# Kernel tuning notes

Hardware: AMD Instinct MI355X
Metric: run time of the kernel (lower is better)

The kernel has to match this reference:

```python
import jax, jax.numpy as jnp
import numpy as np

D_STATE = 16

def setup_inputs() -> dict:
    key = jax.random.key(0)
    ks = jax.random.split(key, 7)
    B, L, d_model = 2, 4096, 1024
    d_inner, d_conv, d_state = 2048, 4, D_STATE
    s = 0.02
    return {
        "x": jax.random.normal(ks[0], (B, L, d_model), jnp.float32),
        "W_in": jax.random.normal(ks[1], (2 * d_inner, d_model), jnp.float32) * s,
        "conv_w": jax.random.normal(ks[2], (d_inner, d_conv), jnp.float32) * 0.3,
        "conv_b": jax.random.normal(ks[3], (d_inner,), jnp.float32) * 0.1,
        "W_xproj": jax.random.normal(ks[4], (2 * d_state + d_inner, d_inner), jnp.float32) * s,
        "D": jnp.ones((d_inner,), jnp.float32),
        "W_out": jax.random.normal(ks[5], (d_model, d_inner), jnp.float32) * s,
    }

def _silu(v):
    return v * jax.nn.sigmoid(v)

def reference(x, W_in, conv_w, conv_b, W_xproj, D, W_out):
    Bsz, L, _ = x.shape
    d_inner, d_conv = conv_w.shape
    d_state = D_STATE
    # in_proj -> split into x branch and gate z
    xz = jnp.einsum('bld,ed->ble', x, W_in)           # [B,L,2*d_inner]
    xb, z = xz[..., :d_inner], xz[..., d_inner:]
    # causal depthwise conv1d (left pad d_conv-1, truncate to L)
    xpad = jnp.pad(xb, ((0, 0), (d_conv - 1, 0), (0, 0)))
    xc = conv_b
    for k in range(d_conv):  # tiny fixed kernel loop
        xc = xc + conv_w[:, k] * xpad[:, k:k + L, :]
    xc = _silu(xc)                                    # [B,L,d_inner]
    # x_proj -> B, C, delta
    proj = jnp.einsum('bld,ed->ble', xc, W_xproj)     # [B,L,2*d_state+d_inner]
    Bm = proj[..., :d_state]
    Cm = proj[..., d_state:2 * d_state]
    delta = jax.nn.softplus(proj[..., 2 * d_state:])  # [B,L,d_inner]
    # selective 'scan' as written collapses: y[b,l,d] = delta*x * sum_s B*C + D*x
    bc = jnp.einsum('bls,bls->bl', Bm, Cm)            # [B,L]
    y = delta * xc * bc[..., None] + D * xc
    y = y * _silu(z)
    return jnp.einsum('bld,ed->ble', y, W_out)        # [B,L,d_model]
```

## Files before the change

### kernel.cpp

```cpp
#include <hip/hip_runtime.h>
#include <hip/hip_bf16.h>
#include <cstdint>
#include <cmath>

typedef __bf16 bf16x8 __attribute__((ext_vector_type(8)));
typedef float  f32x4  __attribute__((ext_vector_type(4)));
typedef unsigned short u16x8 __attribute__((ext_vector_type(8)));

#define BT 128
#define BK 64

__device__ __forceinline__ float bf2f(unsigned short h) {
  union { unsigned int u; float f; } v; v.u = ((unsigned int)h) << 16;
  return v.f;
}
__device__ __forceinline__ unsigned short f2bf(float x) {
  union { float f; unsigned int u; } v; v.f = x;
  unsigned int r = v.u + 0x7fffu + ((v.u >> 16) & 1u);
  return (unsigned short)(r >> 16);
}

__device__ __forceinline__ void gld_lds16(const void* g, void* l) {
  __builtin_amdgcn_global_load_lds(
      (const __attribute__((address_space(1))) unsigned int*)g,
      (__attribute__((address_space(3))) unsigned int*)l,
      16, 0, 0);
}

__device__ __forceinline__ void cvt4(const float* __restrict__ in,
                                     unsigned short* __restrict__ out, int i) {
  float4 v = reinterpret_cast<const float4*>(in)[i];
  ushort4 o;
  o.x = f2bf(v.x); o.y = f2bf(v.y); o.z = f2bf(v.z); o.w = f2bf(v.w);
  reinterpret_cast<ushort4*>(out)[i] = o;
}

__global__ void cvt_head(const float* __restrict__ x, unsigned short* __restrict__ xb,
                         const float* __restrict__ W_in, unsigned short* __restrict__ wb) {
  int b = blockIdx.x;
  if (b < 8192) cvt4(x, xb, b * 256 + threadIdx.x);
  else          cvt4(W_in, wb, (b - 8192) * 256 + threadIdx.x);
}

__device__ void conv_strip(const unsigned short* __restrict__ xz,
                           const float* __restrict__ conv_w,
                           const float* __restrict__ conv_b,
                           unsigned short* __restrict__ xc,
                           int strip, int tid) {
  const int bl0  = strip * 32;
  const int seq0 = bl0 & ~4095;
  const int c0   = tid * 8;
  float w[4][8], bb[8];
#pragma unroll
  for (int j = 0; j < 8; ++j) {
    float4 wr = reinterpret_cast<const float4*>(conv_w)[c0 + j];
    w[0][j] = wr.x; w[1][j] = wr.y; w[2][j] = wr.z; w[3][j] = wr.w;
    bb[j] = conv_b[c0 + j];
  }
  float win[3][8];
#pragma unroll
  for (int i = 0; i < 3; ++i) {
    int r = bl0 - 3 + i;
    if (r >= seq0) {
      u16x8 v = *reinterpret_cast<const u16x8*>(xz + (size_t)r * 4096 + c0);
#pragma unroll
      for (int j = 0; j < 8; ++j) win[i][j] = bf2f(v[j]);
    } else {
#pragma unroll
      for (int j = 0; j < 8; ++j) win[i][j] = 0.f;
    }
  }
  for (int i = 0; i < 32; ++i) {
    const int bl = bl0 + i;
    u16x8 v = *reinterpret_cast<const u16x8*>(xz + (size_t)bl * 4096 + c0);
    u16x8 o;
#pragma unroll
    for (int j = 0; j < 8; ++j) {
      float cur = bf2f(v[j]);
      float a = bb[j] + w[0][j] * win[0][j] + w[1][j] * win[1][j]
                      + w[2][j] * win[2][j] + w[3][j] * cur;
      o[j] = f2bf(a / (1.f + __expf(-a)));
      win[0][j] = win[1][j]; win[1][j] = win[2][j]; win[2][j] = cur;
    }
    *reinterpret_cast<u16x8*>(xc + (size_t)bl * 2048 + c0) = o;
  }
}

__global__ void mid_fused(const unsigned short* __restrict__ xz,
                          const float* __restrict__ conv_w,
                          const float* __restrict__ conv_b,
                          unsigned short* __restrict__ xc,
                          const float* __restrict__ W_xproj, unsigned short* __restrict__ wx_bf,
                          const float* __restrict__ W_out,   unsigned short* __restrict__ wo_bf) {
  int b = blockIdx.x;
  if (b < 256) { conv_strip(xz, conv_w, conv_b, xc, b, threadIdx.x); return; }
  b -= 256;
  if (b < 4160) { cvt4(W_xproj, wx_bf, b * 256 + threadIdx.x); return; }
  cvt4(W_out, wo_bf, (b - 4160) * 256 + threadIdx.x);
}

template <int GUARD_N, int OUT_F32>
__global__ __launch_bounds__(256, 2)
void gemm_bt(const unsigned short* __restrict__ A,
             const unsigned short* __restrict__ B,
             void* __restrict__ Cv,
             int N, int K, int ldA, int ldB, int ldC)
{
  __shared__ __align__(16) unsigned short sA[BT * BK];
  __shared__ __align__(16) unsigned short sB[BT * BK];

  const int tid  = threadIdx.x;
  const int lane = tid & 63;
  const int wave = tid >> 6;
  const int row0 = blockIdx.x * BT;
  const int col0 = blockIdx.y * BT;

  const int wrow = (wave & 1) * 64;
  const int wcol = (wave >> 1) * 64;
  const int l15  = lane & 15;
  const int q    = lane >> 4;

  f32x4 acc[4][4];
#pragma unroll
  for (int i = 0; i < 4; ++i)
#pragma unroll
    for (int j = 0; j < 4; ++j)
      acc[i][j] = (f32x4){0.f, 0.f, 0.f, 0.f};

  const int nk = K / BK;
  for (int kt = 0; kt < nk; ++kt) {
    const int k0 = kt * BK;
#pragma unroll
    for (int t = 0; t < 4; ++t) {
      int c  = t * 256 + tid;
      int r  = c >> 3;
      int g  = c & 7;
      int gs = (g ^ (r & 7)) * 8;
      gld_lds16(A + (size_t)(row0 + r) * ldA + k0 + gs, (void*)(sA + c * 8));
      int br = col0 + r;
      if (GUARD_N) br = (br < N) ? br : (N - 1);
      gld_lds16(B + (size_t)br * ldB + k0 + gs, (void*)(sB + c * 8));
    }
    __syncthreads();

#pragma unroll
    for (int kk = 0; kk < BK; kk += 32) {
      const int grb = kk >> 3;
      bf16x8 af[4], bfr[4];
#pragma unroll
      for (int i = 0; i < 4; ++i) {
        int ar = wrow + i * 16 + l15;
        af[i] = *reinterpret_cast<const bf16x8*>(
            sA + ar * BK + (((grb + q) ^ (ar & 7)) << 3));
        int br = wcol + i * 16 + l15;
        bfr[i] = *reinterpret_cast<const bf16x8*>(
            sB + br * BK + (((grb + q) ^ (br & 7)) << 3));
      }
#pragma unroll
      for (int i = 0; i < 4; ++i)
#pragma unroll
        for (int j = 0; j < 4; ++j)
          acc[i][j] = __builtin_amdgcn_mfma_f32_16x16x32_bf16(af[i], bfr[j], acc[i][j], 0, 0, 0);
    }
    __syncthreads();
  }

#pragma unroll
  for (int i = 0; i < 4; ++i) {
#pragma unroll
    for (int j = 0; j < 4; ++j) {
      int colw = col0 + wcol + j * 16 + l15;
      if (GUARD_N && colw >= N) continue;
#pragma unroll
      for (int r = 0; r < 4; ++r) {
        int roww = row0 + wrow + i * 16 + q * 4 + r;
        if (OUT_F32)
          ((float*)Cv)[(size_t)roww * ldC + colw] = acc[i][j][r];
        else
          ((unsigned short*)Cv)[(size_t)roww * ldC + colw] = f2bf(acc[i][j][r]);
      }
    }
  }
}

#define BARX() do { __builtin_amdgcn_sched_barrier(0); \
                    __builtin_amdgcn_s_barrier(); \
                    __builtin_amdgcn_sched_barrier(0); } while (0)
#define VMW(n) asm volatile("s_waitcnt vmcnt(" #n ")" ::: "memory")
#define LGKM0() asm volatile("s_waitcnt lgkmcnt(0)" ::: "memory")

#define STAGE_A(b, h, kt) do { \
  const unsigned short* _p = Ab + (size_t)((h) * 128) * ldA + (kt) * 64; \
  gld_lds16(_p,                     (void*)&sA[b][((h) * 128      + rr) * 64 + (g8 << 3)]); \
  gld_lds16(_p + (size_t)64 * ldA,  (void*)&sA[b][((h) * 128 + 64 + rr) * 64 + (g8 << 3)]); \
} while (0)

#define STAGE_B(b, h, kt) do { \
  const unsigned short* _p = Bb + (size_t)((h) * 128) * ldB + (kt) * 64; \
  gld_lds16(_p,                     (void*)&sB[b][((h) * 128      + rr) * 64 + (g8 << 3)]); \
  gld_lds16(_p + (size_t)64 * ldB,  (void*)&sB[b][((h) * 128 + 64 + rr) * 64 + (g8 << 3)]); \
} while (0)

#define RD_A_SET(dst, b, p) do { \
  dst[0][0] = *reinterpret_cast<const bf16x8*>(&sA[b][aOff + (2*(p)    ) * 1024 + kph0]); \
  dst[0][1] = *reinterpret_cast<const bf16x8*>(&sA[b][aOff + (2*(p)    ) * 1024 + kph1]); \
  dst[1][0] = *reinterpret_cast<const bf16x8*>(&sA[b][aOff + (2*(p) + 1) * 1024 + kph0]); \
  dst[1][1] = *reinterpret_cast<const bf16x8*>(&sA[b][aOff + (2*(p) + 1) * 1024 + kph1]); \
} while (0)

#define RD_B_SET(dst, b) do { \
  dst[0][0] = *reinterpret_cast<const bf16x8*>(&sB[b][bOff + 0 * 1024 + kph0]); \
  dst[0][1] = *reinterpret_cast<const bf16x8*>(&sB[b][bOff + 0 * 1024 + kph1]); \
  dst[1][0] = *reinterpret_cast<const bf16x8*>(&sB[b][bOff + 1 * 1024 + kph0]); \
  dst[1][1] = *reinterpret_cast<const bf16x8*>(&sB[b][bOff + 1 * 1024 + kph1]); \
  dst[2][0] = *reinterpret_cast<const bf16x8*>(&sB[b][bOff + 2 * 1024 + kph0]); \
  dst[2][1] = *reinterpret_cast<const bf16x8*>(&sB[b][bOff + 2 * 1024 + kph1]); \
  dst[3][0] = *reinterpret_cast<const bf16x8*>(&sB[b][bOff + 3 * 1024 + kph0]); \
  dst[3][1] = *reinterpret_cast<const bf16x8*>(&sB[b][bOff + 3 * 1024 + kph1]); \
} while (0)

#define MMA(i, j, k, Af, Bf) \
  acc[i][j] = __builtin_amdgcn_mfma_f32_16x16x32_bf16(Af[(i) & 1][k], Bf[j][k], acc[i][j], 0, 0, 0)

#define MFMA_PH(p, Af, Bf) do { \
  __builtin_amdgcn_s_setprio(1); \
  MMA(2*(p),   0, 0, Af, Bf); MMA(2*(p),   1, 0, Af, Bf); \
  MMA(2*(p),   2, 0, Af, Bf); MMA(2*(p),   3, 0, Af, Bf); \
  MMA(2*(p)+1, 0, 0, Af, Bf); MMA(2*(p)+1, 1, 0, Af, Bf); \
  MMA(2*(p)+1, 2, 0, Af, Bf); MMA(2*(p)+1, 3, 0, Af, Bf); \
  MMA(2*(p),   0, 1, Af, Bf); MMA(2*(p),   1, 1, Af, Bf); \
  MMA(2*(p),   2, 1, Af, Bf); MMA(2*(p),   3, 1, Af, Bf); \
  MMA(2*(p)+1, 0, 1, Af, Bf); MMA(2*(p)+1, 1, 1, Af, Bf); \
  MMA(2*(p)+1, 2, 1, Af, Bf); MMA(2*(p)+1, 3, 1, Af, Bf); \
  __builtin_amdgcn_s_setprio(0); \
} while (0)

__global__ __launch_bounds__(512, 2)
void gemm256(const unsigned short* __restrict__ A,
             const unsigned short* __restrict__ B,
             unsigned short* __restrict__ C,
             int K, int ldA, int ldB, int ldC, int ccsh)
{
  __shared__ __align__(16) unsigned short smem[4 * 256 * 64];
  unsigned short (*sA)[256 * 64] = (unsigned short (*)[256 * 64])smem;
  unsigned short (*sB)[256 * 64] = (unsigned short (*)[256 * 64])(smem + 2 * 256 * 64);

  const int tid  = threadIdx.x;
  const int lane = tid & 63;
  const int wave = tid >> 6;
  const int wm = wave >> 2;
  const int wn = wave & 3;
  const int l15 = lane & 15;
  const int q   = lane >> 4;

  const int nwg = gridDim.x;
  const int wg  = blockIdx.x;
  const int x   = wg & 7;
  const int c   = wg >> 3;
  const int CC  = 1 << ccsh;
  const int R   = (nwg >> 3) >> ccsh;
  const int row0 = ((x >> 1) * R + (c >> ccsh)) * 256;
  const int col0 = ((x & 1) * CC + (c & (CC - 1))) * 256;

  const int rr  = tid >> 3;
  const int g8  = tid & 7;
  const int gsw = ((g8 ^ (rr & 7)) << 3);
  const unsigned short* Ab = A + (size_t)(row0 + rr) * ldA + gsw;
  const unsigned short* Bb = B + (size_t)(col0 + rr) * ldB + gsw;

  const int aOff = (wm * 128 + l15) * 64;
  const int bOff = (wn * 64  + l15) * 64;
  const int a7   = l15 & 7;
  const int kph0 = ((q       ^ a7) << 3);
  const int kph1 = (((4 + q) ^ a7) << 3);

  f32x4 acc[8][4];
#pragma unroll
  for (int i = 0; i < 8; ++i)
#pragma unroll
    for (int j = 0; j < 4; ++j)
      acc[i][j] = (f32x4){0.f, 0.f, 0.f, 0.f};

  bf16x8 afe[2][2], afo[2][2];
  bf16x8 bfe[4][2], bfo[4][2];

  const int nk = K >> 6;
  STAGE_A(0, 0, 0); STAGE_A(0, 1, 0);
  STAGE_B(0, 0, 0); STAGE_B(0, 1, 0);
  STAGE_B(1, 0, 1); STAGE_B(1, 1, 1);
  VMW(4);
  BARX();
  RD_B_SET(bfe, 0); RD_A_SET(afe, 0, 0);

  const int niter = K >> 7;
  for (int it = 0; it < niter; ++it) {
    const int kt1 = 2 * it + 1;
    int ktE = 2 * it + 2; if (ktE > nk - 1) ktE = nk - 1;
    int ktO = 2 * it + 3; if (ktO > nk - 1) ktO = nk - 1;

    STAGE_A(1, 0, kt1);
    BARX();
    MFMA_PH(0, afe, bfe); RD_A_SET(afo, 0, 1);
    BARX();
    STAGE_A(1, 1, kt1);
    BARX();
    MFMA_PH(1, afo, bfe); RD_A_SET(afe, 0, 2);
    BARX();
    STAGE_B(0, 0, ktE);
    BARX();
    MFMA_PH(2, afe, bfe); RD_A_SET(afo, 0, 3);
    BARX();
    STAGE_B(0, 1, ktE);
    VMW(4);
    BARX();
    MFMA_PH(3, afo, bfe); RD_B_SET(bfo, 1); RD_A_SET(afe, 1, 0);
    BARX();

    STAGE_A(0, 0, ktE);
    BARX();
    MFMA_PH(0, afe, bfo); RD_A_SET(afo, 1, 1);
    BARX();
    STAGE_A(0, 1, ktE);
    BARX();
    MFMA_PH(1, afo, bfo); RD_A_SET(afe, 1, 2);
    BARX();
    STAGE_B(1, 0, ktO);
    BARX();
    MFMA_PH(2, afe, bfo); RD_A_SET(afo, 1, 3);
    BARX();
    STAGE_B(1, 1, ktO);
    VMW(4);
    BARX();
    MFMA_PH(3, afo, bfo); RD_B_SET(bfe, 0); RD_A_SET(afe, 0, 0);
    BARX();
  }

  VMW(0);
  LGKM0();
  BARX();
  {
    unsigned short* cs = smem;
#pragma unroll
    for (int i = 0; i < 8; ++i) {
      const int row = wm * 128 + i * 16 + q * 4;
#pragma unroll
      for (int j = 0; j < 4; ++j) {
        const int col = wn * 64 + j * 16 + l15;
#pragma unroll
        for (int r = 0; r < 4; ++r)
          cs[(row + r) * 256 + col] = f2bf(acc[i][j][r]);
      }
    }
    LGKM0();
    BARX();
#pragma unroll
    for (int s = 0; s < 16; ++s) {
      const int u   = s * 4096 + tid * 8;
      const int row = u >> 8;
      const int col = u & 255;
      u16x8 v = *reinterpret_cast<const u16x8*>(&cs[u]);
      *reinterpret_cast<u16x8*>(C + (size_t)(row0 + row) * ldC + col0 + col) = v;
    }
  }
}

__global__ __launch_bounds__(256)
void proj_strip(const unsigned short* __restrict__ xc,
                const unsigned short* __restrict__ wx,
                unsigned short* __restrict__ proj)
{
  __shared__ float red[4][32 * 32];
  const int tid  = threadIdx.x;
  const int lane = tid & 63;
  const int wave = tid >> 6;
  const int l15  = lane & 15;
  const int q    = lane >> 4;
  const int row0 = blockIdx.x * 32;

  f32x4 acc[2][2];
#pragma unroll
  for (int i = 0; i < 2; ++i)
#pragma unroll
    for (int j = 0; j < 2; ++j) acc[i][j] = (f32x4){0.f, 0.f, 0.f, 0.f};

  const int kbase = wave * 512;
#pragma unroll 4
  for (int kk = 0; kk < 512; kk += 32) {
    const int k = kbase + kk + q * 8;
    bf16x8 a0 = *reinterpret_cast<const bf16x8*>(&xc[(size_t)(row0 + l15) * 2048 + k]);
    bf16x8 a1 = *reinterpret_cast<const bf16x8*>(&xc[(size_t)(row0 + 16 + l15) * 2048 + k]);
    bf16x8 b0 = *reinterpret_cast<const bf16x8*>(&wx[(size_t)(l15) * 2048 + k]);
    bf16x8 b1 = *reinterpret_cast<const bf16x8*>(&wx[(size_t)(16 + l15) * 2048 + k]);
    acc[0][0] = __builtin_amdgcn_mfma_f32_16x16x32_bf16(a0, b0, acc[0][0], 0, 0, 0);
    acc[0][1] = __builtin_amdgcn_mfma_f32_16x16x32_bf16(a0, b1, acc[0][1], 0, 0, 0);
    acc[1][0] = __builtin_amdgcn_mfma_f32_16x16x32_bf16(a1, b0, acc[1][0], 0, 0, 0);
    acc[1][1] = __builtin_amdgcn_mfma_f32_16x16x32_bf16(a1, b1, acc[1][1], 0, 0, 0);
  }

#pragma unroll
  for (int i = 0; i < 2; ++i)
#pragma unroll
    for (int j = 0; j < 2; ++j)
#pragma unroll
      for (int r = 0; r < 4; ++r)
        red[wave][(i * 16 + q * 4 + r) * 32 + j * 16 + l15] = acc[i][j][r];
  __syncthreads();

#pragma unroll
  for (int t = 0; t < 4; ++t) {
    int idx = tid + t * 256;
    float s = red[0][idx] + red[1][idx] + red[2][idx] + red[3][idx];
    proj[(size_t)(row0 + (idx >> 5)) * 2080 + (idx & 31)] = f2bf(s);
  }
}

__global__ void gate_kernel(const unsigned short* __restrict__ proj,
                            const unsigned short* __restrict__ xz,
                            const float* __restrict__ Dw,
                            unsigned short* __restrict__ xc_y)
{
  const int bl = blockIdx.x;
  const unsigned short* p = proj + (size_t)bl * 2080;
  u16x8 pb0 = *reinterpret_cast<const u16x8*>(p);
  u16x8 pb1 = *reinterpret_cast<const u16x8*>(p + 8);
  u16x8 pc0 = *reinterpret_cast<const u16x8*>(p + 16);
  u16x8 pc1 = *reinterpret_cast<const u16x8*>(p + 24);
  float bc = 0.f;
#pragma unroll
  for (int s = 0; s < 8; ++s)
    bc += bf2f(pb0[s]) * bf2f(pc0[s]) + bf2f(pb1[s]) * bf2f(pc1[s]);

  const int c0 = threadIdx.x * 8;
  u16x8 dv  = *reinterpret_cast<const u16x8*>(p + 32 + c0);
  u16x8 xcv = *reinterpret_cast<const u16x8*>(xc_y + (size_t)bl * 2048 + c0);
  u16x8 zv  = *reinterpret_cast<const u16x8*>(xz + (size_t)bl * 4096 + 2048 + c0);
  float4 d0 = reinterpret_cast<const float4*>(Dw)[c0 / 4];
  float4 d1 = reinterpret_cast<const float4*>(Dw)[c0 / 4 + 1];
  const float* dd0 = reinterpret_cast<const float*>(&d0);
  const float* dd1 = reinterpret_cast<const float*>(&d1);

  u16x8 o;
#pragma unroll
  for (int j = 0; j < 8; ++j) {
    float d = bf2f(dv[j]);
    float delta = (d > 15.f) ? d : __logf(1.f + __expf(d));
    float xv = bf2f(xcv[j]);
    float z  = bf2f(zv[j]);
    float Dj = (j < 4) ? dd0[j] : dd1[j - 4];
    float y = delta * xv * bc + Dj * xv;
    y *= z / (1.f + __expf(-z));
    o[j] = f2bf(y);
  }
  *reinterpret_cast<u16x8*>(xc_y + (size_t)bl * 2048 + c0) = o;
}

extern "C" void kernel_launch(void* const* d_in, const int* in_sizes, int n_in,
                              void* d_out, int out_size, void* d_ws, size_t ws_size,
                              hipStream_t stream) {
  const float* x       = (const float*)d_in[0];
  const float* W_in    = (const float*)d_in[1];
  const float* conv_w  = (const float*)d_in[2];
  const float* conv_b  = (const float*)d_in[3];
  const float* W_xproj = (const float*)d_in[4];
  const float* Dw      = (const float*)d_in[5];
  const float* W_out   = (const float*)d_in[6];
  float* out = (float*)d_out;

  unsigned short* xz_bf   = (unsigned short*)d_ws;
  unsigned short* xc_bf   = xz_bf  + (size_t)8192 * 4096;
  unsigned short* proj_bf = xc_bf  + (size_t)8192 * 2048;
  unsigned short* xb_bf   = proj_bf + (size_t)8192 * 2080;
  unsigned short* w_bf    = xb_bf  + (size_t)8192 * 1024;

  cvt_head<<<8192 + 4096, 256, 0, stream>>>(x, xb_bf, W_in, w_bf);
  gemm256<<<512, 512, 0, stream>>>(xb_bf, w_bf, xz_bf, 1024, 1024, 1024, 4096, 3);
  mid_fused<<<256 + 4160 + 2048, 256, 0, stream>>>(xz_bf, conv_w, conv_b, xc_bf,
                                                   W_xproj, xb_bf, W_out, w_bf);
  proj_strip<<<256, 256, 0, stream>>>(xc_bf, xb_bf, proj_bf);
  gemm256<<<256, 512, 0, stream>>>(xc_bf, xb_bf + (size_t)32 * 2048, proj_bf + 32,
                                   2048, 2048, 2048, 2080, 2);
  gate_kernel<<<8192, 256, 0, stream>>>(proj_bf, xz_bf, Dw, xc_bf);
  gemm_bt<0, 1><<<dim3(64, 8), 256, 0, stream>>>(xc_bf, w_bf, out, 1024, 2048, 2048, 2048, 1024);
}
```

Baseline: 343.9 us.

## Halve barriers in GEMM main loop and swizzle epilogue LDS stores

Restructures the double-buffered GEMM main loop so each phase issues its global-to-LDS stages, then the next fragment's LDS reads, then the MFMA phase. This removes roughly half of the workgroup barriers and lets the LDS reads overlap with the matrix math. It also XOR-swizzles the column index in the bf16 epilogue staging buffer to cut LDS bank conflicts on the scattered stores. With fewer barriers, the code depends on the remaining ones still ordering LDS buffer reuse correctly, and a mistake there would be a race.

New measurement: 355.5 us. +3.4%, slower.

```diff
diff --git a/kernel.cpp b/kernel.cpp
--- a/kernel.cpp
+++ b/kernel.cpp
@@ -294,45 +294,35 @@
 
   const int niter = K >> 7;
   for (int it = 0; it < niter; ++it) {
-    const int kt1 = 2 * it + 1;
-    int ktE = 2 * it + 2; if (ktE > nk - 1) ktE = nk - 1;
-    int ktO = 2 * it + 3; if (ktO > nk - 1) ktO = nk - 1;
-
-    STAGE_A(1, 0, kt1);
-    BARX();
-    MFMA_PH(0, afe, bfe); RD_A_SET(afo, 0, 1);
-    BARX();
-    STAGE_A(1, 1, kt1);
-    BARX();
-    MFMA_PH(1, afo, bfe); RD_A_SET(afe, 0, 2);
-    BARX();
-    STAGE_B(0, 0, ktE);
-    BARX();
-    MFMA_PH(2, afe, bfe); RD_A_SET(afo, 0, 3);
-    BARX();
-    STAGE_B(0, 1, ktE);
+    const int ktA0 = 2 * it + 1;
+    int kt2 = 2 * it + 2; if (kt2 > nk - 1) kt2 = nk - 1;
+    int kt3 = 2 * it + 3; if (kt3 > nk - 1) kt3 = nk - 1;
+
+    BARX();
+    STAGE_A(1, 0, ktA0);
+    RD_A_SET(afo, 0, 1); MFMA_PH(0, afe, bfe);
+    BARX();
+    STAGE_A(1, 1, ktA0); STAGE_B(0, 0, kt2);
+    RD_A_SET(afe, 0, 2); MFMA_PH(1, afo, bfe);
+    BARX();
+    STAGE_B(0, 1, kt2);
+    RD_A_SET(afo, 0, 3); MFMA_PH(2, afe, bfe);
     VMW(4);
     BARX();
-    MFMA_PH(3, afo, bfe); RD_B_SET(bfo, 1); RD_A_SET(afe, 1, 0);
-    BARX();
-
-    STAGE_A(0, 0, ktE);
-    BARX();
-    MFMA_PH(0, afe, bfo); RD_A_SET(afo, 1, 1);
-    BARX();
-    STAGE_A(0, 1, ktE);
-    BARX();
-    MFMA_PH(1, afo, bfo); RD_A_SET(afe, 1, 2);
-    BARX();
-    STAGE_B(1, 0, ktO);
-    BARX();
-    MFMA_PH(2, afe, bfo); RD_A_SET(afo, 1, 3);
-    BARX();
-    STAGE_B(1, 1, ktO);
+    RD_B_SET(bfo, 1); RD_A_SET(afe, 1, 0); MFMA_PH(3, afo, bfe);
+
+    BARX();
+    STAGE_A(0, 0, kt2);
+    RD_A_SET(afo, 1, 1); MFMA_PH(0, afe, bfo);
+    BARX();
+    STAGE_A(0, 1, kt2); STAGE_B(1, 0, kt3);
+    RD_A_SET(afe, 1, 2); MFMA_PH(1, afo, bfo);
+    BARX();
+    STAGE_B(1, 1, kt3);
+    RD_A_SET(afo, 1, 3); MFMA_PH(2, afe, bfo);
     VMW(4);
     BARX();
-    MFMA_PH(3, afo, bfo); RD_B_SET(bfe, 0); RD_A_SET(afe, 0, 0);
-    BARX();
+    RD_B_SET(bfe, 0); RD_A_SET(afe, 0, 0); MFMA_PH(3, afo, bfo);
   }
 
   VMW(0);
@@ -345,7 +335,7 @@
       const int row = wm * 128 + i * 16 + q * 4;
 #pragma unroll
       for (int j = 0; j < 4; ++j) {
-        const int col = wn * 64 + j * 16 + l15;
+        const int col = (wn * 64 + j * 16 + l15) ^ (q << 4);
 #pragma unroll
         for (int r = 0; r < 4; ++r)
           cs[(row + r) * 256 + col] = f2bf(acc[i][j][r]);
@@ -358,7 +348,8 @@
       const int u   = s * 4096 + tid * 8;
       const int row = u >> 8;
       const int col = u & 255;
-      u16x8 v = *reinterpret_cast<const u16x8*>(&cs[u]);
+      const int rcol = col ^ (((row >> 2) & 3) << 4);
+      u16x8 v = *reinterpret_cast<const u16x8*>(&cs[row * 256 + rcol]);
       *reinterpret_cast<u16x8*>(C + (size_t)(row0 + row) * ldC + col0 + col) = v;
     }
   }
```
